# Kernel tuning notes

Measured on AMD Instinct MI355X. Metric: run time of the kernel, lower is better.

## Reference

```python
import jax, jax.numpy as jnp
import numpy as np

N = 50000      # total nodes (actors) across batch
E = 300000     # edges surviving the distance threshold
N_AGT = 128    # n_actor
N_CTX = 128    # n_ctx == n_actor for A2A
EPS = 1e-5


def _gn(x, gamma, beta):
    # torch GroupNorm(num_groups=1) on a [N, C] tensor: normalize over C per row
    mu = jnp.mean(x, axis=-1, keepdims=True)
    var = jnp.mean((x - mu) ** 2, axis=-1, keepdims=True)
    return (x - mu) * jax.lax.rsqrt(var + EPS) * gamma + beta


def setup_inputs() -> dict:
    key = jax.random.key(0)
    ks = jax.random.split(key, 16)
    s = 0.02
    f32 = jnp.float32
    inp = {
        'agts': jax.random.normal(ks[0], (N, N_AGT), f32),
        'ctx': jax.random.normal(ks[1], (N, N_CTX), f32),
        'agt_ctrs': jax.random.normal(ks[2], (N, 2), f32),
        'ctx_ctrs': jax.random.normal(ks[3], (N, 2), f32),
        'hi': jax.random.randint(ks[4], (E,), 0, N, dtype=jnp.int32),
        'wi': jax.random.randint(ks[5], (E,), 0, N, dtype=jnp.int32),
        # dist: nn.Linear(2, n_ctx) -> ReLU -> Linear(n_ctx, n_ctx, GN, act)
        'w_d1': jax.random.normal(ks[6], (N_CTX, 2), f32) * s,
        'b_d1': jnp.zeros((N_CTX,), f32),
        'w_d2': jax.random.normal(ks[7], (N_CTX, N_CTX), f32) * s,
        'g_d2': jnp.ones((N_CTX,), f32), 'bt_d2': jnp.zeros((N_CTX,), f32),
        # query: Linear(n_agt, n_ctx, GN, act)
        'w_q': jax.random.normal(ks[8], (N_CTX, N_AGT), f32) * s,
        'g_q': jnp.ones((N_CTX,), f32), 'bt_q': jnp.zeros((N_CTX,), f32),
        # ctx: Linear(3*n_ctx, n_agt, GN, act) -> nn.Linear(n_agt, n_agt, bias=False)
        'w_c1': jax.random.normal(ks[9], (N_AGT, 3 * N_CTX), f32) * s,
        'g_c1': jnp.ones((N_AGT,), f32), 'bt_c1': jnp.zeros((N_AGT,), f32),
        'w_c2': jax.random.normal(ks[10], (N_AGT, N_AGT), f32) * s,
        # agt: nn.Linear(n_agt, n_agt, bias=False)
        'w_a': jax.random.normal(ks[11], (N_AGT, N_AGT), f32) * s,
        # norm: GroupNorm(1, n_agt)
        'g_n': jnp.ones((N_AGT,), f32), 'bt_n': jnp.zeros((N_AGT,), f32),
        # linear: Linear(n_agt, n_agt, GN, act=False)
        'w_l': jax.random.normal(ks[12], (N_AGT, N_AGT), f32) * s,
        'g_l': jnp.ones((N_AGT,), f32), 'bt_l': jnp.zeros((N_AGT,), f32),
    }
    return inp


def reference(agts, ctx, agt_ctrs, ctx_ctrs, hi, wi,
              w_d1, b_d1, w_d2, g_d2, bt_d2,
              w_q, g_q, bt_q,
              w_c1, g_c1, bt_c1, w_c2,
              w_a, g_n, bt_n,
              w_l, g_l, bt_l):
    res = agts
    # edge-wise distance features: [E, 2] -> [E, n_ctx]
    d = agt_ctrs[hi] - ctx_ctrs[wi]
    d = jax.nn.relu(d @ w_d1.T + b_d1)
    d = jax.nn.relu(_gn(d @ w_d2.T, g_d2, bt_d2))
    # edge-wise query from gathered target nodes: [E, n_ctx]
    q = jax.nn.relu(_gn(agts[hi] @ w_q.T, g_q, bt_q))
    # fuse dist/query/context: [E, 3*n_ctx] -> [E, n_agt]
    e = jnp.concatenate([d, q, ctx[wi]], axis=-1)
    e = jax.nn.relu(_gn(e @ w_c1.T, g_c1, bt_c1))
    e = e @ w_c2.T
    # scatter-add messages back to nodes
    out = agts @ w_a.T
    out = out.at[hi].add(e)
    out = jax.nn.relu(_gn(out, g_n, bt_n))
    out = _gn(out @ w_l.T, g_l, bt_l)
    return jax.nn.relu(out + res)
```

## Files before the change

### kernel.cpp

```cpp
#include <hip/hip_runtime.h>
#include <hip/hip_bf16.h>

#define NCH 128
#define EB  32
#define NB  32

typedef __attribute__((ext_vector_type(8))) short bf16x8;
typedef __attribute__((ext_vector_type(4))) float f32x4;

__device__ inline unsigned short f2bf(float v) {
    __hip_bfloat16 h = __float2bfloat16(v);
    return __builtin_bit_cast(unsigned short, h);
}

__device__ inline bf16x8 cvt8(const float* __restrict__ p) {
    bf16x8 r;
#pragma unroll
    for (int i = 0; i < 8; ++i) r[i] = (short)f2bf(p[i]);
    return r;
}

template<bool BF>
__device__ inline bf16x8 load_row8(const void* __restrict__ src, int node, int koff) {
    if constexpr (BF)
        return *(const bf16x8*)((const unsigned short*)src + (size_t)node * NCH + koff);
    else
        return cvt8((const float*)src + (size_t)node * NCH + koff);
}

__global__ __launch_bounds__(256) void convert_weights_kernel(
    const float* __restrict__ w_d2, const float* __restrict__ w_q,
    const float* __restrict__ w_c1, const float* __restrict__ w_c2,
    const float* __restrict__ w_a,  const float* __restrict__ w_l,
    unsigned short* __restrict__ out)
{
    int i = blockIdx.x * 256 + threadIdx.x;
    const float* src; int off;
    if      (i < 16384)  { src = w_d2; off = i; }
    else if (i < 32768)  { src = w_q;  off = i - 16384; }
    else if (i < 81920)  { src = w_c1; off = i - 32768; }
    else if (i < 98304)  { src = w_c2; off = i - 81920; }
    else if (i < 114688) { src = w_a;  off = i - 98304; }
    else if (i < 131072) { src = w_l;  off = i - 114688; }
    else return;
    out[i] = f2bf(src[off]);
}

__global__ __launch_bounds__(256) void convert_nodes_kernel(
    const float* __restrict__ a, const float* __restrict__ c,
    unsigned short* __restrict__ abf, unsigned short* __restrict__ cbf, int nq)
{
    const int stride = gridDim.x * blockDim.x;
    for (int i = blockIdx.x * blockDim.x + threadIdx.x; i < 2 * nq; i += stride) {
        const bool isa = i < nq;
        const int j = isa ? i : i - nq;
        float4 v = (isa ? (const float4*)a : (const float4*)c)[j];
        ushort4 o = { f2bf(v.x), f2bf(v.y), f2bf(v.z), f2bf(v.w) };
        (isa ? (ushort4*)abf : (ushort4*)cbf)[j] = o;
    }
}

__device__ inline void gemm_k128_lds(const unsigned short* __restrict__ A,
                                     const unsigned short* __restrict__ W,
                                     int lane, int wave, f32x4 (&acc)[2][2])
{
#pragma unroll
    for (int k = 0; k < 4; ++k) {
        const int koff = k * 32 + (lane >> 4) * 8;
        bf16x8 a[2], b[2];
#pragma unroll
        for (int m = 0; m < 2; ++m) {
            int r = m * 16 + (lane & 15);
            int byte = (r * 256 + koff * 2) ^ ((r & 7) << 4);
            a[m] = *(const bf16x8*)((const char*)A + byte);
        }
#pragma unroll
        for (int n = 0; n < 2; ++n) {
            int wr = wave * 32 + n * 16 + (lane & 15);
            b[n] = *(const bf16x8*)(W + (size_t)wr * NCH + koff);
        }
#pragma unroll
        for (int m = 0; m < 2; ++m)
#pragma unroll
            for (int n = 0; n < 2; ++n)
                acc[m][n] = __builtin_amdgcn_mfma_f32_16x16x32_bf16(a[m], b[n], acc[m][n], 0, 0, 0);
    }
}

__device__ inline void gn_frag_stats(const f32x4 (&acc)[2][2],
                                     float (*red_s)[4], float (*red_q)[4],
                                     int t, float (&mu)[2][4], float (&rs)[2][4])
{
    const int lane = t & 63, wave = t >> 6;
    float s[2][4], q[2][4];
#pragma unroll
    for (int m = 0; m < 2; ++m)
#pragma unroll
        for (int j = 0; j < 4; ++j) {
            float sv = acc[m][0][j] + acc[m][1][j];
            float qv = acc[m][0][j] * acc[m][0][j] + acc[m][1][j] * acc[m][1][j];
#pragma unroll
            for (int off = 1; off < 16; off <<= 1) {
                sv += __shfl_xor(sv, off);
                qv += __shfl_xor(qv, off);
            }
            s[m][j] = sv; q[m][j] = qv;
        }
    if ((lane & 15) == 0) {
        const int rg = lane >> 4;
#pragma unroll
        for (int m = 0; m < 2; ++m)
#pragma unroll
            for (int j = 0; j < 4; ++j) {
                int r = m * 16 + rg * 4 + j;
                red_s[r][wave] = s[m][j];
                red_q[r][wave] = q[m][j];
            }
    }
    __syncthreads();
#pragma unroll
    for (int m = 0; m < 2; ++m)
#pragma unroll
        for (int j = 0; j < 4; ++j) {
            int r = m * 16 + ((lane >> 4) << 2) + j;
            float4 sv = *(const float4*)red_s[r];
            float4 qv = *(const float4*)red_q[r];
            float ssum = (sv.x + sv.y) + (sv.z + sv.w);
            float qsum = (qv.x + qv.y) + (qv.z + qv.w);
            float m_  = ssum * (1.f / NCH);
            float var = qsum * (1.f / NCH) - m_ * m_;
            mu[m][j] = m_;
            rs[m][j] = rsqrtf(var + 1e-5f);
        }
}

__device__ inline void gn_pack_store(const f32x4 (&acc)[2][2],
                                     const float (&mu)[2][4], const float (&rs)[2][4],
                                     const float* __restrict__ gamma,
                                     const float* __restrict__ beta,
                                     unsigned short* __restrict__ dst, int t)
{
    const int lane = t & 63, wave = t >> 6;
    const int c0 = wave * 32 + (lane & 15);
    const float g0 = gamma[c0],      b0 = beta[c0];
    const float g1 = gamma[c0 + 16], b1 = beta[c0 + 16];
#pragma unroll
    for (int m = 0; m < 2; ++m)
#pragma unroll
        for (int j = 0; j < 4; ++j) {
            int r = m * 16 + ((lane >> 4) << 2) + j;
            float v0 = fmaxf((acc[m][0][j] - mu[m][j]) * rs[m][j] * g0 + b0, 0.f);
            float v1 = fmaxf((acc[m][1][j] - mu[m][j]) * rs[m][j] * g1 + b1, 0.f);
            unsigned int p0 = f2bf(v0), p1 = f2bf(v1);
            unsigned int o0 = (unsigned int)__shfl_xor((int)p0, 1);
            unsigned int o1 = (unsigned int)__shfl_xor((int)p1, 1);
            if (!(lane & 1)) {
                int cb = c0 * 2;
                int byte0 = (r * 256 + cb) ^ ((r & 7) << 4);
                int byte1 = (r * 256 + cb + 32) ^ ((r & 7) << 4);
                *(unsigned int*)((char*)dst + byte0) = (p0 & 0xffffu) | (o0 << 16);
                *(unsigned int*)((char*)dst + byte1) = (p1 & 0xffffu) | (o1 << 16);
            }
        }
    __syncthreads();
}

template<bool BF>
__global__ __launch_bounds__(256) void edge_kernel(
    const void* __restrict__ agts_nb, const void* __restrict__ ctx_nb,
    const float* __restrict__ agt_ctrs, const float* __restrict__ ctx_ctrs,
    const int* __restrict__ hi, const int* __restrict__ wi,
    const float* __restrict__ w_d1, const float* __restrict__ b_d1,
    const float* __restrict__ g_d2, const float* __restrict__ bt_d2,
    const float* __restrict__ g_q, const float* __restrict__ bt_q,
    const float* __restrict__ g_c1, const float* __restrict__ bt_c1,
    const unsigned short* __restrict__ wbf,
    float* __restrict__ outbuf, int E)
{
    const int t = threadIdx.x;
    const int lane = t & 63;
    const int wave = t >> 6;
    const int e0 = blockIdx.x * EB;

    __shared__ unsigned short bfA[EB * NCH];
    __shared__ unsigned short bfD[EB * NCH];
    __shared__ unsigned short bfX[EB * NCH];
    __shared__ __align__(16) float red_s[EB][4];
    __shared__ __align__(16) float red_q[EB][4];
    __shared__ int   sh_h[EB], sh_w[EB];
    __shared__ float sh_dx[EB], sh_dy[EB];

    const unsigned short* Wd2 = wbf;
    const unsigned short* Wq  = wbf + 16384;
    const unsigned short* Wc1 = wbf + 32768;
    const unsigned short* Wc2 = wbf + 81920;

    if (t < EB) {
        int e = e0 + t; if (e >= E) e = E - 1;
        int h = hi[e], w = wi[e];
        sh_h[t] = h; sh_w[t] = w;
        sh_dx[t] = agt_ctrs[2 * h]     - ctx_ctrs[2 * w];
        sh_dy[t] = agt_ctrs[2 * h + 1] - ctx_ctrs[2 * w + 1];
    }
    __syncthreads();

    {
        const int r  = t >> 3;
        const int cc = t & 7;
        const int h = sh_h[r], w = sh_w[r];
#pragma unroll
        for (int half = 0; half < 2; ++half) {
            int c = cc + half * 8;
            bf16x8 av = load_row8<BF>(agts_nb, h, c * 8);
            bf16x8 xv = load_row8<BF>(ctx_nb,  w, c * 8);
            int byte = (r * 256 + c * 16) ^ ((r & 7) << 4);
            *(bf16x8*)((char*)bfA + byte) = av;
            *(bf16x8*)((char*)bfX + byte) = xv;
        }
    }
    {
        const int c = t & 127, rh = t >> 7;
        const float wa = w_d1[2 * c], wb = w_d1[2 * c + 1], bb = b_d1[c];
#pragma unroll
        for (int i = 0; i < 16; ++i) {
            int r = rh * 16 + i;
            float v = fmaxf(fmaf(wa, sh_dx[r], fmaf(wb, sh_dy[r], bb)), 0.f);
            unsigned int pv = f2bf(v);
            unsigned int ov = (unsigned int)__shfl_xor((int)pv, 1);
            if (!(c & 1)) {
                int byte = (r * 256 + c * 2) ^ ((r & 7) << 4);
                *(unsigned int*)((char*)bfD + byte) = (pv & 0xffffu) | (ov << 16);
            }
        }
    }
    __syncthreads();

    const f32x4 z = { 0.f, 0.f, 0.f, 0.f };
    f32x4 acc[2][2];
    float mu[2][4], rs[2][4];

    acc[0][0] = z; acc[0][1] = z; acc[1][0] = z; acc[1][1] = z;
    gemm_k128_lds(bfD, Wd2, lane, wave, acc);
    gn_frag_stats(acc, red_s, red_q, t, mu, rs);
    gn_pack_store(acc, mu, rs, g_d2, bt_d2, bfD, t);

    acc[0][0] = z; acc[0][1] = z; acc[1][0] = z; acc[1][1] = z;
    gemm_k128_lds(bfA, Wq, lane, wave, acc);
    gn_frag_stats(acc, red_s, red_q, t, mu, rs);
    gn_pack_store(acc, mu, rs, g_q, bt_q, bfA, t);

    acc[0][0] = z; acc[0][1] = z; acc[1][0] = z; acc[1][1] = z;
#pragma unroll
    for (int kt = 0; kt < 12; ++kt) {
        const unsigned short* Ab = (kt < 4) ? bfD : (kt < 8) ? bfA : bfX;
        const int koff = (kt & 3) * 32 + (lane >> 4) * 8;
        bf16x8 a[2], b[2];
#pragma unroll
        for (int m = 0; m < 2; ++m) {
            int r = m * 16 + (lane & 15);
            int byte = (r * 256 + koff * 2) ^ ((r & 7) << 4);
            a[m] = *(const bf16x8*)((const char*)Ab + byte);
        }
#pragma unroll
        for (int n = 0; n < 2; ++n) {
            int wr = wave * 32 + n * 16 + (lane & 15);
            b[n] = *(const bf16x8*)(Wc1 + (size_t)wr * 384 + kt * 32 + (lane >> 4) * 8);
        }
#pragma unroll
        for (int m = 0; m < 2; ++m)
#pragma unroll
            for (int n = 0; n < 2; ++n)
                acc[m][n] = __builtin_amdgcn_mfma_f32_16x16x32_bf16(a[m], b[n], acc[m][n], 0, 0, 0);
    }
    gn_frag_stats(acc, red_s, red_q, t, mu, rs);
    gn_pack_store(acc, mu, rs, g_c1, bt_c1, bfD, t);

    acc[0][0] = z; acc[0][1] = z; acc[1][0] = z; acc[1][1] = z;
    gemm_k128_lds(bfD, Wc2, lane, wave, acc);
#pragma unroll
    for (int m = 0; m < 2; ++m)
#pragma unroll
        for (int n = 0; n < 2; ++n)
#pragma unroll
            for (int j = 0; j < 4; ++j) {
                int r = m * 16 + ((lane >> 4) << 2) + j;
                if (e0 + r < E)
                    atomicAdd(&outbuf[(size_t)sh_h[r] * NCH + wave * 32 + n * 16 + (lane & 15)],
                              acc[m][n][j]);
            }
}

template<bool BF>
__global__ __launch_bounds__(256) void node_init_kernel(
    const void* __restrict__ agts_nb, const unsigned short* __restrict__ wa_bf,
    float* __restrict__ outbuf, int N)
{
    const int t = threadIdx.x;
    const int lane = t & 63, wave = t >> 6;
    const int n0 = blockIdx.x * NB;

    int r0 = n0 + (lane & 15);      if (r0 >= N) r0 = N - 1;
    int r1 = n0 + 16 + (lane & 15); if (r1 >= N) r1 = N - 1;

    const f32x4 z = { 0.f, 0.f, 0.f, 0.f };
    f32x4 acc[2][2] = { { z, z }, { z, z } };
#pragma unroll
    for (int k = 0; k < 4; ++k) {
        const int koff = k * 32 + (lane >> 4) * 8;
        bf16x8 a[2], b[2];
        a[0] = load_row8<BF>(agts_nb, r0, koff);
        a[1] = load_row8<BF>(agts_nb, r1, koff);
#pragma unroll
        for (int n = 0; n < 2; ++n) {
            int wr = wave * 32 + n * 16 + (lane & 15);
            b[n] = *(const bf16x8*)(wa_bf + (size_t)wr * NCH + koff);
        }
#pragma unroll
        for (int m = 0; m < 2; ++m)
#pragma unroll
            for (int n = 0; n < 2; ++n)
                acc[m][n] = __builtin_amdgcn_mfma_f32_16x16x32_bf16(a[m], b[n], acc[m][n], 0, 0, 0);
    }
#pragma unroll
    for (int m = 0; m < 2; ++m)
#pragma unroll
        for (int n = 0; n < 2; ++n)
#pragma unroll
            for (int j = 0; j < 4; ++j) {
                int r = m * 16 + ((lane >> 4) << 2) + j;
                int ng = n0 + r;
                if (ng < N)
                    outbuf[(size_t)ng * NCH + wave * 32 + n * 16 + (lane & 15)] = acc[m][n][j];
            }
}

__global__ __launch_bounds__(256) void node_post_kernel(
    float* __restrict__ outbuf, const float* __restrict__ agts,
    const float* __restrict__ g_n, const float* __restrict__ bt_n,
    const unsigned short* __restrict__ wl_bf,
    const float* __restrict__ g_l, const float* __restrict__ bt_l, int N)
{
    const int t = threadIdx.x;
    const int lane = t & 63, wave = t >> 6;
    const int n0 = blockIdx.x * NB;

    __shared__ unsigned short bfP[NB * NCH];
    __shared__ __align__(16) float red_s[NB][4];
    __shared__ __align__(16) float red_q[NB][4];

    const int c = t & 127, rh = t >> 7;
    float v[16];
#pragma unroll
    for (int i = 0; i < 16; ++i) {
        int n = n0 + rh * 16 + i; if (n >= N) n = N - 1;
        v[i] = outbuf[(size_t)n * NCH + c];
    }
#pragma unroll
    for (int i = 0; i < 16; ++i) {
        float s = v[i], q = v[i] * v[i];
        for (int off = 32; off > 0; off >>= 1) {
            s += __shfl_down(s, off);
            q += __shfl_down(q, off);
        }
        if (lane == 0) { red_s[rh * 16 + i][wave & 1] = s; red_q[rh * 16 + i][wave & 1] = q; }
    }
    __syncthreads();
    {
        const float g = g_n[c], b = bt_n[c];
#pragma unroll
        for (int i = 0; i < 16; ++i) {
            int r = rh * 16 + i;
            float s = red_s[r][0] + red_s[r][1];
            float q = red_q[r][0] + red_q[r][1];
            float m_  = s * (1.f / NCH);
            float var = q * (1.f / NCH) - m_ * m_;
            float rrs = rsqrtf(var + 1e-5f);
            float val = fmaxf((v[i] - m_) * rrs * g + b, 0.f);
            unsigned int pv = f2bf(val);
            unsigned int ov = (unsigned int)__shfl_xor((int)pv, 1);
            if (!(c & 1)) {
                int byte = (r * 256 + c * 2) ^ ((r & 7) << 4);
                *(unsigned int*)((char*)bfP + byte) = (pv & 0xffffu) | (ov << 16);
            }
        }
    }
    __syncthreads();

    const f32x4 z = { 0.f, 0.f, 0.f, 0.f };
    f32x4 acc[2][2] = { { z, z }, { z, z } };
    gemm_k128_lds(bfP, wl_bf, lane, wave, acc);

    float mu[2][4], rs[2][4];
    gn_frag_stats(acc, red_s, red_q, t, mu, rs);
    const int c0 = wave * 32 + (lane & 15);
    const float g0 = g_l[c0],      b0 = bt_l[c0];
    const float g1 = g_l[c0 + 16], b1 = bt_l[c0 + 16];
#pragma unroll
    for (int m = 0; m < 2; ++m)
#pragma unroll
        for (int j = 0; j < 4; ++j) {
            int r = m * 16 + ((lane >> 4) << 2) + j;
            int ng = n0 + r;
            if (ng < N) {
                float v0 = (acc[m][0][j] - mu[m][j]) * rs[m][j] * g0 + b0;
                float v1 = (acc[m][1][j] - mu[m][j]) * rs[m][j] * g1 + b1;
                v0 = fmaxf(v0 + agts[(size_t)ng * NCH + c0], 0.f);
                v1 = fmaxf(v1 + agts[(size_t)ng * NCH + c0 + 16], 0.f);
                outbuf[(size_t)ng * NCH + c0]      = v0;
                outbuf[(size_t)ng * NCH + c0 + 16] = v1;
            }
        }
}

extern "C" void kernel_launch(void* const* d_in, const int* in_sizes, int n_in,
                              void* d_out, int out_size, void* d_ws, size_t ws_size,
                              hipStream_t stream) {
    const float* agts     = (const float*)d_in[0];
    const float* ctx      = (const float*)d_in[1];
    const float* agt_ctrs = (const float*)d_in[2];
    const float* ctx_ctrs = (const float*)d_in[3];
    const int*   hi       = (const int*)d_in[4];
    const int*   wi       = (const int*)d_in[5];
    const float* w_d1     = (const float*)d_in[6];
    const float* b_d1     = (const float*)d_in[7];
    const float* w_d2     = (const float*)d_in[8];
    const float* g_d2     = (const float*)d_in[9];
    const float* bt_d2    = (const float*)d_in[10];
    const float* w_q      = (const float*)d_in[11];
    const float* g_q      = (const float*)d_in[12];
    const float* bt_q     = (const float*)d_in[13];
    const float* w_c1     = (const float*)d_in[14];
    const float* g_c1     = (const float*)d_in[15];
    const float* bt_c1    = (const float*)d_in[16];
    const float* w_c2     = (const float*)d_in[17];
    const float* w_a      = (const float*)d_in[18];
    const float* g_n      = (const float*)d_in[19];
    const float* bt_n     = (const float*)d_in[20];
    const float* w_l      = (const float*)d_in[21];
    const float* g_l      = (const float*)d_in[22];
    const float* bt_l     = (const float*)d_in[23];

    const int N = in_sizes[0] / NCH;
    const int E = in_sizes[4];

    float* outbuf = (float*)d_out;

    unsigned short* wbf = (unsigned short*)d_ws;
    unsigned short* abf = wbf + 131072;
    unsigned short* cbf = abf + (size_t)N * NCH;
    const size_t need = 262144ull + (size_t)N * NCH * 4ull;
    const bool big = (d_ws != nullptr) && (ws_size >= need);

    const int nb_nodes = (N + NB - 1) / NB;
    const int nb_edges = (E + EB - 1) / EB;

    convert_weights_kernel<<<512, 256, 0, stream>>>(w_d2, w_q, w_c1, w_c2, w_a, w_l, wbf);

    if (big) {
        convert_nodes_kernel<<<2048, 256, 0, stream>>>(agts, ctx, abf, cbf, N * NCH / 4);
        node_init_kernel<true><<<nb_nodes, 256, 0, stream>>>(abf, wbf + 98304, outbuf, N);
        edge_kernel<true><<<nb_edges, 256, 0, stream>>>(
            abf, cbf, agt_ctrs, ctx_ctrs, hi, wi,
            w_d1, b_d1, g_d2, bt_d2, g_q, bt_q, g_c1, bt_c1,
            wbf, outbuf, E);
    } else {
        node_init_kernel<false><<<nb_nodes, 256, 0, stream>>>(agts, wbf + 98304, outbuf, N);
        edge_kernel<false><<<nb_edges, 256, 0, stream>>>(
            agts, ctx, agt_ctrs, ctx_ctrs, hi, wi,
            w_d1, b_d1, g_d2, bt_d2, g_q, bt_q, g_c1, bt_c1,
            wbf, outbuf, E);
    }
    node_post_kernel<<<nb_nodes, 256, 0, stream>>>(
        outbuf, agts, g_n, bt_n, wbf + 114688, g_l, bt_l, N);
}
```

Baseline: 366.7 us.

## Precompute per-node query projection once instead of per edge

```diff
diff --git a/kernel.cpp b/kernel.cpp
--- a/kernel.cpp
+++ b/kernel.cpp
@@ -46,17 +46,14 @@
     out[i] = f2bf(src[off]);
 }
 
-__global__ __launch_bounds__(256) void convert_nodes_kernel(
-    const float* __restrict__ a, const float* __restrict__ c,
-    unsigned short* __restrict__ abf, unsigned short* __restrict__ cbf, int nq)
+__global__ __launch_bounds__(256) void convert_ctx_kernel(
+    const float* __restrict__ c, unsigned short* __restrict__ cbf, int nq)
 {
     const int stride = gridDim.x * blockDim.x;
-    for (int i = blockIdx.x * blockDim.x + threadIdx.x; i < 2 * nq; i += stride) {
-        const bool isa = i < nq;
-        const int j = isa ? i : i - nq;
-        float4 v = (isa ? (const float4*)a : (const float4*)c)[j];
+    for (int i = blockIdx.x * blockDim.x + threadIdx.x; i < nq; i += stride) {
+        float4 v = ((const float4*)c)[i];
         ushort4 o = { f2bf(v.x), f2bf(v.y), f2bf(v.z), f2bf(v.w) };
-        (isa ? (ushort4*)abf : (ushort4*)cbf)[j] = o;
+        ((ushort4*)cbf)[i] = o;
     }
 }
 
@@ -165,9 +162,83 @@
     __syncthreads();
 }
 
-template<bool BF>
+__global__ __launch_bounds__(256) void node_prep_kernel(
+    const float* __restrict__ agts,
+    const unsigned short* __restrict__ wa_bf, const unsigned short* __restrict__ wq_bf,
+    const float* __restrict__ g_q, const float* __restrict__ bt_q,
+    float* __restrict__ outbuf, unsigned short* __restrict__ qbf, int N)
+{
+    const int t = threadIdx.x;
+    const int lane = t & 63, wave = t >> 6;
+    const int n0 = blockIdx.x * NB;
+
+    __shared__ __align__(16) float red_s[NB][4];
+    __shared__ __align__(16) float red_q[NB][4];
+
+    int r0 = n0 + (lane & 15);      if (r0 >= N) r0 = N - 1;
+    int r1 = n0 + 16 + (lane & 15); if (r1 >= N) r1 = N - 1;
+
+    const f32x4 z = { 0.f, 0.f, 0.f, 0.f };
+    f32x4 accO[2][2] = { { z, z }, { z, z } };
+    f32x4 accQ[2][2] = { { z, z }, { z, z } };
+#pragma unroll
+    for (int k = 0; k < 4; ++k) {
+        const int koff = k * 32 + (lane >> 4) * 8;
+        bf16x8 a[2], bo[2], bq[2];
+        a[0] = load_row8<false>(agts, r0, koff);
+        a[1] = load_row8<false>(agts, r1, koff);
+#pragma unroll
+        for (int n = 0; n < 2; ++n) {
+            int wr = wave * 32 + n * 16 + (lane & 15);
+            bo[n] = *(const bf16x8*)(wa_bf + (size_t)wr * NCH + koff);
+            bq[n] = *(const bf16x8*)(wq_bf + (size_t)wr * NCH + koff);
+        }
+#pragma unroll
+        for (int m = 0; m < 2; ++m)
+#pragma unroll
+            for (int n = 0; n < 2; ++n) {
+                accO[m][n] = __builtin_amdgcn_mfma_f32_16x16x32_bf16(a[m], bo[n], accO[m][n], 0, 0, 0);
+                accQ[m][n] = __builtin_amdgcn_mfma_f32_16x16x32_bf16(a[m], bq[n], accQ[m][n], 0, 0, 0);
+            }
+    }
+#pragma unroll
+    for (int m = 0; m < 2; ++m)
+#pragma unroll
+        for (int n = 0; n < 2; ++n)
+#pragma unroll
+            for (int j = 0; j < 4; ++j) {
+                int r = m * 16 + ((lane >> 4) << 2) + j;
+                int ng = n0 + r;
+                if (ng < N)
+                    outbuf[(size_t)ng * NCH + wave * 32 + n * 16 + (lane & 15)] = accO[m][n][j];
+            }
+    float mu[2][4], rs[2][4];
+    gn_frag_stats(accQ, red_s, red_q, t, mu, rs);
+    const int c0 = wave * 32 + (lane & 15);
+    const float g0 = g_q[c0],      b0 = bt_q[c0];
+    const float g1 = g_q[c0 + 16], b1 = bt_q[c0 + 16];
+#pragma unroll
+    for (int m = 0; m < 2; ++m)
+#pragma unroll
+        for (int j = 0; j < 4; ++j) {
+            int r = m * 16 + ((lane >> 4) << 2) + j;
+            int ng = n0 + r;
+            float v0 = fmaxf((accQ[m][0][j] - mu[m][j]) * rs[m][j] * g0 + b0, 0.f);
+            float v1 = fmaxf((accQ[m][1][j] - mu[m][j]) * rs[m][j] * g1 + b1, 0.f);
+            unsigned int p0 = f2bf(v0), p1 = f2bf(v1);
+            unsigned int o0 = (unsigned int)__shfl_xor((int)p0, 1);
+            unsigned int o1 = (unsigned int)__shfl_xor((int)p1, 1);
+            if (!(lane & 1) && ng < N) {
+                unsigned int* rowp = (unsigned int*)((char*)qbf + (size_t)ng * 256);
+                rowp[c0 >> 1]        = (p0 & 0xffffu) | (o0 << 16);
+                rowp[(c0 + 16) >> 1] = (p1 & 0xffffu) | (o1 << 16);
+            }
+        }
+}
+
+template<bool BIG>
 __global__ __launch_bounds__(256) void edge_kernel(
-    const void* __restrict__ agts_nb, const void* __restrict__ ctx_nb,
+    const void* __restrict__ qsrc, const void* __restrict__ ctx_nb,
     const float* __restrict__ agt_ctrs, const float* __restrict__ ctx_ctrs,
     const int* __restrict__ hi, const int* __restrict__ wi,
     const float* __restrict__ w_d1, const float* __restrict__ b_d1,
@@ -182,7 +253,7 @@
     const int wave = t >> 6;
     const int e0 = blockIdx.x * EB;
 
-    __shared__ unsigned short bfA[EB * NCH];
+    __shared__ unsigned short bfQ[EB * NCH];
     __shared__ unsigned short bfD[EB * NCH];
     __shared__ unsigned short bfX[EB * NCH];
     __shared__ __align__(16) float red_s[EB][4];
@@ -211,10 +282,10 @@
 #pragma unroll
         for (int half = 0; half < 2; ++half) {
             int c = cc + half * 8;
-            bf16x8 av = load_row8<BF>(agts_nb, h, c * 8);
-            bf16x8 xv = load_row8<BF>(ctx_nb,  w, c * 8);
+            bf16x8 qv = load_row8<BIG>(qsrc, h, c * 8);
+            bf16x8 xv = load_row8<BIG>(ctx_nb, w, c * 8);
             int byte = (r * 256 + c * 16) ^ ((r & 7) << 4);
-            *(bf16x8*)((char*)bfA + byte) = av;
+            *(bf16x8*)((char*)bfQ + byte) = qv;
             *(bf16x8*)((char*)bfX + byte) = xv;
         }
     }
@@ -244,15 +315,17 @@
     gn_frag_stats(acc, red_s, red_q, t, mu, rs);
     gn_pack_store(acc, mu, rs, g_d2, bt_d2, bfD, t);
 
+    if constexpr (!BIG) {
+        acc[0][0] = z; acc[0][1] = z; acc[1][0] = z; acc[1][1] = z;
+        gemm_k128_lds(bfQ, Wq, lane, wave, acc);
+        gn_frag_stats(acc, red_s, red_q, t, mu, rs);
+        gn_pack_store(acc, mu, rs, g_q, bt_q, bfQ, t);
+    }
+
     acc[0][0] = z; acc[0][1] = z; acc[1][0] = z; acc[1][1] = z;
-    gemm_k128_lds(bfA, Wq, lane, wave, acc);
-    gn_frag_stats(acc, red_s, red_q, t, mu, rs);
-    gn_pack_store(acc, mu, rs, g_q, bt_q, bfA, t);
-
-    acc[0][0] = z; acc[0][1] = z; acc[1][0] = z; acc[1][1] = z;
 #pragma unroll
     for (int kt = 0; kt < 12; ++kt) {
-        const unsigned short* Ab = (kt < 4) ? bfD : (kt < 8) ? bfA : bfX;
+        const unsigned short* Ab = (kt < 4) ? bfD : (kt < 8) ? bfQ : bfX;
         const int koff = (kt & 3) * 32 + (lane >> 4) * 8;
         bf16x8 a[2], b[2];
 #pragma unroll
@@ -290,9 +363,8 @@
             }
 }
 
-template<bool BF>
 __global__ __launch_bounds__(256) void node_init_kernel(
-    const void* __restrict__ agts_nb, const unsigned short* __restrict__ wa_bf,
+    const float* __restrict__ agts, const unsigned short* __restrict__ wa_bf,
     float* __restrict__ outbuf, int N)
 {
     const int t = threadIdx.x;
@@ -308,8 +380,8 @@
     for (int k = 0; k < 4; ++k) {
         const int koff = k * 32 + (lane >> 4) * 8;
         bf16x8 a[2], b[2];
-        a[0] = load_row8<BF>(agts_nb, r0, koff);
-        a[1] = load_row8<BF>(agts_nb, r1, koff);
+        a[0] = load_row8<false>(agts, r0, koff);
+        a[1] = load_row8<false>(agts, r1, koff);
 #pragma unroll
         for (int n = 0; n < 2; ++n) {
             int wr = wave * 32 + n * 16 + (lane & 15);
@@ -446,8 +518,8 @@
     float* outbuf = (float*)d_out;
 
     unsigned short* wbf = (unsigned short*)d_ws;
-    unsigned short* abf = wbf + 131072;
-    unsigned short* cbf = abf + (size_t)N * NCH;
+    unsigned short* cbf = wbf + 131072;
+    unsigned short* qbf = cbf + (size_t)N * NCH;
     const size_t need = 262144ull + (size_t)N * NCH * 4ull;
     const bool big = (d_ws != nullptr) && (ws_size >= need);
 
@@ -457,14 +529,15 @@
     convert_weights_kernel<<<512, 256, 0, stream>>>(w_d2, w_q, w_c1, w_c2, w_a, w_l, wbf);
 
     if (big) {
-        convert_nodes_kernel<<<2048, 256, 0, stream>>>(agts, ctx, abf, cbf, N * NCH / 4);
-        node_init_kernel<true><<<nb_nodes, 256, 0, stream>>>(abf, wbf + 98304, outbuf, N);
+        convert_ctx_kernel<<<1024, 256, 0, stream>>>(ctx, cbf, N * NCH / 4);
+        node_prep_kernel<<<nb_nodes, 256, 0, stream>>>(
+            agts, wbf + 98304, wbf + 16384, g_q, bt_q, outbuf, qbf, N);
         edge_kernel<true><<<nb_edges, 256, 0, stream>>>(
-            abf, cbf, agt_ctrs, ctx_ctrs, hi, wi,
+            qbf, cbf, agt_ctrs, ctx_ctrs, hi, wi,
             w_d1, b_d1, g_d2, bt_d2, g_q, bt_q, g_c1, bt_c1,
             wbf, outbuf, E);
     } else {
-        node_init_kernel<false><<<nb_nodes, 256, 0, stream>>>(agts, wbf + 98304, outbuf, N);
+        node_init_kernel<<<nb_nodes, 256, 0, stream>>>(agts, wbf + 98304, outbuf, N);
         edge_kernel<false><<<nb_edges, 256, 0, stream>>>(
             agts, ctx, agt_ctrs, ctx_ctrs, hi, wi,
             w_d1, b_d1, g_d2, bt_d2, g_q, bt_q, g_c1, bt_c1,
```

Result: faster. 325.7 us (-11.2%).
